# Performance work log

Measured on AMD Instinct MI355X. Metric: run time of the kernel, lower is better.

The kernel has to match this reference:

```python
import jax, jax.numpy as jnp
import numpy as np

N_NODES = 50000
N_EDGES = 625000
D = 128          # hidden_dim
H = 8            # num_heads
DH = D // H      # head_dim
L = 4            # num_layers
F_IN = 64        # in_channels
G = 64           # num graphs
BETA = 1.0
EPS = 1e-5       # layernorm eps


def _seg_softmax(s, idx, n):
    # softmax of s over segments defined by idx (segments present in idx are never empty)
    m = jax.ops.segment_max(s, idx, num_segments=n)
    e = jnp.exp(s - m[idx])
    d = jax.ops.segment_sum(e, idx, num_segments=n)
    return e / d[idx]


def _ln(x, s, b):
    mu = jnp.mean(x, axis=-1, keepdims=True)
    var = jnp.var(x, axis=-1, keepdims=True)
    return (x - mu) / jnp.sqrt(var + EPS) * s + b


def _forward(x, edge_index, batch, node_W, node_b, cW1, cb1, cW2, cb2,
             qW, qb, kW, kb, vW, vb, oW, ob, bW, bb,
             f1W, f1b, f2W, f2b, n1s, n1b, n2s, n2b,
             outW1, outb1, outW2, outb2):
    N = x.shape[0]
    src, tgt = edge_index[0], edge_index[1]
    h = x @ node_W + node_b                              # [N, D]
    for l in range(L):
        # ---- dynamic curvature (attention-approximated Wasserstein) ----
        h_src, h_tgt = h[src], h[tgt]                    # [E, D]
        sim = jnp.sum(h_src * h_tgt, axis=-1) * BETA     # [E]
        alpha = _seg_softmax(sim, tgt, N)                # segment softmax over tgt
        dist = jnp.linalg.norm(h_src - h_tgt, axis=-1)   # [E]
        agg = jax.ops.segment_sum(alpha * dist, tgt, num_segments=N)
        curv = 1.0 - agg[tgt] / jnp.maximum(dist, 1e-6)  # [E]
        ce = jax.nn.relu(curv[:, None] @ cW1 + cb1) @ cW2 + cb2  # [E, D]
        # ---- CurvphormerLayer ----
        xn = _ln(h, n1s[l], n1b[l])
        q = (xn @ qW[l] + qb[l]).reshape(N, H, DH)
        k = (xn @ kW[l] + kb[l]).reshape(N, H, DH)
        v = (xn @ vW[l] + vb[l]).reshape(N, H, DH)
        scores = jnp.sum(q[src] * k[tgt], axis=-1) / (DH ** 0.5)  # [E, H]
        scores = scores + ce @ bW[l] + bb[l]                       # curvature bias
        probs = _seg_softmax(scores, tgt, N)                       # [E, H]
        msgs = (probs[..., None] * v[tgt]).reshape(-1, D)          # [E, D]
        aggm = jax.ops.segment_sum(msgs, src, num_segments=N)     # scatter to src
        h = h + (aggm @ oW[l] + ob[l])
        xn2 = _ln(h, n2s[l], n2b[l])
        h = h + (jax.nn.relu(xn2 @ f1W[l] + f1b[l]) @ f2W[l] + f2b[l])
    # ---- mean pool per graph ----
    counts = jnp.maximum(jax.ops.segment_sum(jnp.ones((N,), h.dtype), batch, num_segments=G), 1.0)
    g = jax.ops.segment_sum(h, batch, num_segments=G) / counts[:, None]
    return jax.nn.relu(g @ outW1 + outb1) @ outW2 + outb2


def setup_inputs() -> dict:
    keys = iter(jax.random.split(jax.random.key(0), 32))
    p = lambda shape, s=0.02: jax.random.normal(next(keys), shape, jnp.float32) * s
    x = jax.random.normal(next(keys), (N_NODES, F_IN), jnp.float32)
    edge_index = jax.random.randint(next(keys), (2, N_EDGES), 0, N_NODES)
    batch = jnp.sort(jax.random.randint(next(keys), (N_NODES,), 0, G))
    inp = {
        "x": x, "edge_index": edge_index, "batch": batch,
        "node_W": p((F_IN, D)), "node_b": p((D,)),
        "cW1": p((1, D)), "cb1": p((D,)), "cW2": p((D, D)), "cb2": p((D,)),
        "qW": p((L, D, D)), "qb": p((L, D)),
        "kW": p((L, D, D)), "kb": p((L, D)),
        "vW": p((L, D, D)), "vb": p((L, D)),
        "oW": p((L, D, D)), "ob": p((L, D)),
        "bW": p((L, D, H)), "bb": p((L, H)),
        "f1W": p((L, D, 4 * D)), "f1b": p((L, 4 * D)),
        "f2W": p((L, 4 * D, D)), "f2b": p((L, D)),
        "n1s": jnp.ones((L, D), jnp.float32), "n1b": jnp.zeros((L, D), jnp.float32),
        "n2s": jnp.ones((L, D), jnp.float32), "n2b": jnp.zeros((L, D), jnp.float32),
        "outW1": p((D, D // 2)), "outb1": p((D // 2,)),
        "outW2": p((D // 2, 1)), "outb2": p((1,)),
    }
    return inp


def reference(x, edge_index, batch, node_W, node_b, cW1, cb1, cW2, cb2,
              qW, qb, kW, kb, vW, vb, oW, ob, bW, bb,
              f1W, f1b, f2W, f2b, n1s, n1b, n2s, n2b,
              outW1, outb1, outW2, outb2):
    return _forward(x, edge_index, batch, node_W, node_b, cW1, cb1, cW2, cb2,
                    qW, qb, kW, kb, vW, vb, oW, ob, bW, bb,
                    f1W, f1b, f2W, f2b, n1s, n1b, n2s, n2b,
                    outW1, outb1, outW2, outb2)
```

## Files before the change

kernel.cpp:

```cpp
#include <hip/hip_runtime.h>

#define NN 50000
#define NE 625000
#define DD 128
#define HH 8
#define DHH 16
#define NL 4
#define FIN 64
#define NG 64
#define LN_EPS 1e-5f
#define NSEG 129
#define NT32 1563
#define NT64 782
#define NBS 196
#define HLP 132

typedef __bf16 bf16x8_t __attribute__((ext_vector_type(8)));
typedef unsigned short ushort8_t __attribute__((ext_vector_type(8)));
typedef float f32x4_t __attribute__((ext_vector_type(4)));
union BF8 { ushort8_t u; bf16x8_t b; };

__device__ __forceinline__ void fma4(float4& a, float s, float4 w) {
  a.x = fmaf(s, w.x, a.x); a.y = fmaf(s, w.y, a.y);
  a.z = fmaf(s, w.z, a.z); a.w = fmaf(s, w.w, a.w);
}
__device__ __forceinline__ unsigned short f2bf(float f) {
  unsigned u = __float_as_uint(f);
  unsigned r = ((u >> 16) & 1u) + 0x7FFFu;
  return (unsigned short)((u + r) >> 16);
}
__device__ __forceinline__ float bf2f(unsigned short u) {
  return __uint_as_float((unsigned)u << 16);
}

__device__ __forceinline__ void ln_tile_bf32(const float* __restrict__ h, int nb,
                                             const float* __restrict__ sc,
                                             const float* __restrict__ bi,
                                             ushort* xbf) {
  int tid = threadIdx.x;
  int r = tid >> 4, l16 = tid & 15;
  int nr = nb + r; if (nr >= NN) nr = NN - 1;
  const float* hp = h + (size_t)nr * DD + l16 * 8;
  float4 a0 = *(const float4*)hp;
  float4 a1 = *(const float4*)(hp + 4);
  float sum = a0.x + a0.y + a0.z + a0.w + a1.x + a1.y + a1.z + a1.w;
  float sq  = a0.x*a0.x + a0.y*a0.y + a0.z*a0.z + a0.w*a0.w
            + a1.x*a1.x + a1.y*a1.y + a1.z*a1.z + a1.w*a1.w;
#pragma unroll
  for (int off = 8; off >= 1; off >>= 1) {
    sum += __shfl_xor(sum, off, 64);
    sq  += __shfl_xor(sq,  off, 64);
  }
  float mu   = sum * (1.0f / DD);
  float var  = sq * (1.0f / DD) - mu * mu;
  float rstd = rsqrtf(var + LN_EPS);
  int d0 = l16 * 8;
  float4 s0 = *(const float4*)(sc + d0), s1 = *(const float4*)(sc + d0 + 4);
  float4 b0 = *(const float4*)(bi + d0), b1 = *(const float4*)(bi + d0 + 4);
  ushort8_t u;
  u[0] = f2bf((a0.x - mu) * rstd * s0.x + b0.x);
  u[1] = f2bf((a0.y - mu) * rstd * s0.y + b0.y);
  u[2] = f2bf((a0.z - mu) * rstd * s0.z + b0.z);
  u[3] = f2bf((a0.w - mu) * rstd * s0.w + b0.w);
  u[4] = f2bf((a1.x - mu) * rstd * s1.x + b1.x);
  u[5] = f2bf((a1.y - mu) * rstd * s1.y + b1.y);
  u[6] = f2bf((a1.z - mu) * rstd * s1.z + b1.z);
  u[7] = f2bf((a1.w - mu) * rstd * s1.w + b1.w);
  int off = (r * 256 + l16 * 16) ^ ((r & 7) << 4);
  *(ushort8_t*)((char*)xbf + off) = u;
}

__global__ __launch_bounds__(256) void k_node_proj(const float* __restrict__ x,
                                                   const float* __restrict__ W,
                                                   const float* __restrict__ b,
                                                   float* __restrict__ h) {
  __shared__ float Wl[FIN * DD];
  __shared__ float xt[32][FIN];
  int tid = threadIdx.x;
  int nb = blockIdx.x * 32;
  for (int i = tid * 4; i < FIN * DD; i += 1024)
    *(float4*)&Wl[i] = *(const float4*)(W + i);
  for (int i = tid * 4; i < 32 * FIN; i += 1024) {
    int row = i >> 6, cc = i & 63;
    int node = nb + row; if (node >= NN) node = NN - 1;
    *(float4*)&xt[row][cc] = *(const float4*)(x + (size_t)node * FIN + cc);
  }
  __syncthreads();
  int c4 = (tid & 31) * 4;
  int r0 = (tid >> 5) * 4;
  float4 bv = *(const float4*)(b + c4);
  float4 a0 = bv, a1 = bv, a2 = bv, a3 = bv;
  for (int k = 0; k < FIN; k++) {
    float4 wv = *(const float4*)&Wl[k * DD + c4];
    fma4(a0, xt[r0][k], wv);
    fma4(a1, xt[r0 + 1][k], wv);
    fma4(a2, xt[r0 + 2][k], wv);
    fma4(a3, xt[r0 + 3][k], wv);
  }
  int n0 = nb + r0;
  if (n0 < NN)     *(float4*)(h + (size_t)n0 * DD + c4) = a0;
  if (n0 + 1 < NN) *(float4*)(h + (size_t)(n0 + 1) * DD + c4) = a1;
  if (n0 + 2 < NN) *(float4*)(h + (size_t)(n0 + 2) * DD + c4) = a2;
  if (n0 + 3 < NN) *(float4*)(h + (size_t)(n0 + 3) * DD + c4) = a3;
}

__global__ __launch_bounds__(256) void k_edge1(const int* __restrict__ src_s, const int* __restrict__ tgt_s,
                                               const float* __restrict__ h, float* __restrict__ sim,
                                               float* __restrict__ dist) {
  int gid = blockIdx.x * 256 + threadIdx.x;
  int e = gid >> 4;
  if (e >= NE) return;
  int j = gid & 15;
  int s = src_s[e], t = tgt_s[e];
  const float4* ap = (const float4*)(h + (size_t)s * DD + j * 8);
  const float4* bp = (const float4*)(h + (size_t)t * DD + j * 8);
  float4 a0 = ap[0], a1 = ap[1];
  float4 b0 = bp[0], b1 = bp[1];
  float dot = 0.f, sq = 0.f;
  dot = fmaf(a0.x, b0.x, dot); dot = fmaf(a0.y, b0.y, dot);
  dot = fmaf(a0.z, b0.z, dot); dot = fmaf(a0.w, b0.w, dot);
  dot = fmaf(a1.x, b1.x, dot); dot = fmaf(a1.y, b1.y, dot);
  dot = fmaf(a1.z, b1.z, dot); dot = fmaf(a1.w, b1.w, dot);
  float d0 = a0.x - b0.x, d1 = a0.y - b0.y, d2 = a0.z - b0.z, d3 = a0.w - b0.w;
  float d4 = a1.x - b1.x, d5 = a1.y - b1.y, d6 = a1.z - b1.z, d7 = a1.w - b1.w;
  sq = fmaf(d0, d0, sq); sq = fmaf(d1, d1, sq); sq = fmaf(d2, d2, sq); sq = fmaf(d3, d3, sq);
  sq = fmaf(d4, d4, sq); sq = fmaf(d5, d5, sq); sq = fmaf(d6, d6, sq); sq = fmaf(d7, d7, sq);
#pragma unroll
  for (int off = 8; off >= 1; off >>= 1) {
    dot += __shfl_xor(dot, off, 64);
    sq  += __shfl_xor(sq,  off, 64);
  }
  if (j == 0) {
    sim[e]  = dot;
    dist[e] = sqrtf(sq);
  }
}

__global__ __launch_bounds__(256) void k_curva(const int* __restrict__ rowstart_t,
    const int* __restrict__ eid_t, const float* __restrict__ sim,
    const float* __restrict__ dist, float* __restrict__ aggv) {
  int node = blockIdx.x * 32 + (threadIdx.x >> 3);
  if (node >= NN) return;
  int j = threadIdx.x & 7;
  int rs = rowstart_t[node], re = rowstart_t[node + 1];
  float m = -3.4e38f;
  for (int i = rs + j; i < re; i += 8) m = fmaxf(m, sim[eid_t[i]]);
#pragma unroll
  for (int off = 1; off <= 4; off <<= 1) m = fmaxf(m, __shfl_xor(m, off, 64));
  float den = 0.f, nd = 0.f;
  for (int i = rs + j; i < re; i += 8) {
    int e = eid_t[i];
    float ev = expf(sim[e] - m);
    den += ev;
    nd = fmaf(ev, dist[e], nd);
  }
#pragma unroll
  for (int off = 1; off <= 4; off <<= 1) {
    den += __shfl_xor(den, off, 64);
    nd  += __shfl_xor(nd,  off, 64);
  }
  if (j == 0) aggv[node] = den > 0.f ? nd / den : 0.f;
}

__global__ __launch_bounds__(512) void k_ln_qkv(const float* __restrict__ h,
    const float* __restrict__ n1s_l, const float* __restrict__ n1b_l,
    const ushort* __restrict__ qkvT_l,
    const float* __restrict__ qb_l, const float* __restrict__ kb_l, const float* __restrict__ vb_l,
    ushort* __restrict__ q, ushort* __restrict__ kk, ushort* __restrict__ v) {
  __shared__ __align__(16) ushort xbf[32 * DD];
  int nb = blockIdx.x * 32;
  ln_tile_bf32(h, nb, n1s_l, n1b_l, xbf);
  __syncthreads();
  int lane = threadIdx.x & 63;
  int w = threadIdx.x >> 6;
  int g = lane >> 4, c = lane & 15;
  int xr = (c & 7) << 4;
  char* xb = (char*)xbf;
  BF8 a[2][4];
#pragma unroll
  for (int nt = 0; nt < 2; nt++)
#pragma unroll
    for (int kt = 0; kt < 4; kt++)
      a[nt][kt].u = *(ushort8_t*)(xb + (((nt * 16 + c) * 256 + kt * 64 + g * 16) ^ xr));
#pragma unroll
  for (int ti = 0; ti < 3; ti++) {
    int t = w * 3 + ti;
    int m = t >> 3;
    int colb = (t & 7) * 16;
    const float* bias = (m == 0 ? qb_l : (m == 1 ? kb_l : vb_l));
    float4 bv = *(const float4*)(bias + colb + g * 4);
    f32x4_t acc0 = {bv.x, bv.y, bv.z, bv.w};
    f32x4_t acc1 = acc0;
    const ushort* wp = qkvT_l + (size_t)(m * DD + colb + c) * DD + g * 8;
#pragma unroll
    for (int kt = 0; kt < 4; kt++) {
      BF8 b; b.u = *(const ushort8_t*)(wp + kt * 32);
      acc0 = __builtin_amdgcn_mfma_f32_16x16x32_bf16(b.b, a[0][kt].b, acc0, 0, 0, 0);
      acc1 = __builtin_amdgcn_mfma_f32_16x16x32_bf16(b.b, a[1][kt].b, acc1, 0, 0, 0);
    }
    ushort* out = (m == 0 ? q : (m == 1 ? kk : v));
    int n0 = nb + c;
    if (n0 < NN) {
      ushort4 o; o.x = f2bf(acc0[0]); o.y = f2bf(acc0[1]); o.z = f2bf(acc0[2]); o.w = f2bf(acc0[3]);
      *(ushort4*)(out + (size_t)n0 * DD + colb + g * 4) = o;
    }
    int n1 = nb + 16 + c;
    if (n1 < NN) {
      ushort4 o; o.x = f2bf(acc1[0]); o.y = f2bf(acc1[1]); o.z = f2bf(acc1[2]); o.w = f2bf(acc1[3]);
      *(ushort4*)(out + (size_t)n1 * DD + colb + g * 4) = o;
    }
  }
}

__global__ __launch_bounds__(256) void k_scores_sm(const int* __restrict__ src_s,
    const int* __restrict__ rowstart_t, const int* __restrict__ eid_t,
    const ushort* __restrict__ q, const ushort* __restrict__ k,
    const float* __restrict__ dist, const float* __restrict__ aggv,
    const float* __restrict__ bp_g,
    const float* __restrict__ slope_l, const float* __restrict__ inter_l,
    float* __restrict__ escore, float2* __restrict__ msd) {
  __shared__ float lsl[NSEG * HH], lin[NSEG * HH], bp[DD];
  int tid = threadIdx.x;
  for (int idx = tid; idx < NSEG * HH; idx += 256) { lsl[idx] = slope_l[idx]; lin[idx] = inter_l[idx]; }
  if (tid < DD) bp[tid] = bp_g[tid];
  __syncthreads();
  int node = blockIdx.x * 32 + (tid >> 3);
  if (node >= NN) return;
  int hh = tid & 7;
  int rs = rowstart_t[node], re = rowstart_t[node + 1];
  float av = aggv[node];
  const ushort8_t* kp = (const ushort8_t*)(k + (size_t)node * DD + hh * DHH);
  ushort8_t k0 = kp[0], k1 = kp[1];
  float m = -3.4e38f;
  int i = rs;
  int e_n = 0, s_n = 0; float dd_n = 0.f; ushort8_t q0_n = {}, q1_n = {};
  if (i < re) {
    e_n = eid_t[i]; s_n = src_s[e_n]; dd_n = dist[e_n];
    const ushort8_t* qp = (const ushort8_t*)(q + (size_t)s_n * DD + hh * DHH);
    q0_n = qp[0]; q1_n = qp[1];
  }
  while (i < re) {
    int e = e_n; float dd = dd_n;
    ushort8_t q0 = q0_n, q1 = q1_n;
    int j = i + 1;
    if (j < re) {
      e_n = eid_t[j]; s_n = src_s[e_n]; dd_n = dist[e_n];
      const ushort8_t* qp = (const ushort8_t*)(q + (size_t)s_n * DD + hh * DHH);
      q0_n = qp[0]; q1_n = qp[1];
    }
    float curv = 1.0f - av / fmaxf(dd, 1e-6f);
    int lo = 0, hi = DD;
    while (lo < hi) { int mid = (lo + hi) >> 1; if (bp[mid] < curv) lo = mid + 1; else hi = mid; }
    float bias = fmaf(lsl[lo * HH + hh], curv, lin[lo * HH + hh]);
    float dot = 0.f;
#pragma unroll
    for (int jj = 0; jj < 8; jj++) dot = fmaf(bf2f(q0[jj]), bf2f(k0[jj]), dot);
#pragma unroll
    for (int jj = 0; jj < 8; jj++) dot = fmaf(bf2f(q1[jj]), bf2f(k1[jj]), dot);
    float sc = dot * 0.25f + bias;
    escore[e * HH + hh] = sc;
    m = fmaxf(m, sc);
    i = j;
  }
  float sum = 0.f;
  for (i = rs; i < re; i++)
    sum += expf(escore[eid_t[i] * HH + hh] - m);
  float2 o; o.x = m; o.y = sum > 0.f ? 1.0f / sum : 0.f;
  msd[(size_t)node * HH + hh] = o;
}

__global__ __launch_bounds__(256) void k_agg(const int* __restrict__ tgt_s,
    const int* __restrict__ rowstart,
    const float* __restrict__ escore, const float2* __restrict__ msd,
    const ushort* __restrict__ v, ushort* __restrict__ aggmb) {
  int wave = (blockIdx.x * 256 + threadIdx.x) >> 6;
  int lane = threadIdx.x & 63;
  int rs = rowstart[wave], re = rowstart[wave + 1];
  int hh = lane >> 3;
  int d = lane * 2;
  float a0 = 0.f, a1 = 0.f;
  int i = rs;
  for (; i + 4 <= re; i += 4) {
    int t0 = tgt_s[i], t1 = tgt_s[i + 1], t2 = tgt_s[i + 2], t3 = tgt_s[i + 3];
    float e0 = escore[(i    ) * HH + hh];
    float e1 = escore[(i + 1) * HH + hh];
    float e2 = escore[(i + 2) * HH + hh];
    float e3 = escore[(i + 3) * HH + hh];
    float2 m0 = msd[(size_t)t0 * HH + hh], m1 = msd[(size_t)t1 * HH + hh];
    float2 m2 = msd[(size_t)t2 * HH + hh], m3 = msd[(size_t)t3 * HH + hh];
    ushort2 v0 = *(const ushort2*)(v + (size_t)t0 * DD + d);
    ushort2 v1 = *(const ushort2*)(v + (size_t)t1 * DD + d);
    ushort2 v2 = *(const ushort2*)(v + (size_t)t2 * DD + d);
    ushort2 v3 = *(const ushort2*)(v + (size_t)t3 * DD + d);
    float p0 = expf(e0 - m0.x) * m0.y;
    float p1 = expf(e1 - m1.x) * m1.y;
    float p2 = expf(e2 - m2.x) * m2.y;
    float p3 = expf(e3 - m3.x) * m3.y;
    a0 = fmaf(p0, bf2f(v0.x), a0); a1 = fmaf(p0, bf2f(v0.y), a1);
    a0 = fmaf(p1, bf2f(v1.x), a0); a1 = fmaf(p1, bf2f(v1.y), a1);
    a0 = fmaf(p2, bf2f(v2.x), a0); a1 = fmaf(p2, bf2f(v2.y), a1);
    a0 = fmaf(p3, bf2f(v3.x), a0); a1 = fmaf(p3, bf2f(v3.y), a1);
  }
  for (; i < re; i++) {
    int t = tgt_s[i];
    float2 md = msd[(size_t)t * HH + hh];
    float prob = expf(escore[i * HH + hh] - md.x) * md.y;
    ushort2 vv = *(const ushort2*)(v + (size_t)t * DD + d);
    a0 = fmaf(prob, bf2f(vv.x), a0);
    a1 = fmaf(prob, bf2f(vv.y), a1);
  }
  ushort2 o; o.x = f2bf(a0); o.y = f2bf(a1);
  *(ushort2*)(aggmb + (size_t)wave * DD + d) = o;
}

__global__ __launch_bounds__(512) void k_attn_ffn(const ushort* __restrict__ aggmb,
    const ushort* __restrict__ oT_l, const float* __restrict__ ob_l,
    const float* __restrict__ n2s_l, const float* __restrict__ n2b_l,
    const ushort* __restrict__ f1T_l, const float* __restrict__ f1b_l,
    const ushort* __restrict__ f2T_l, const float* __restrict__ f2b_l,
    float* __restrict__ h) {
  __shared__ float hL[64 * HLP];
  __shared__ __align__(16) char ubuf[64 * 256 * 2];
  char* xb = ubuf;
  char* tb = ubuf;
  int nb = blockIdx.x * 64;
  int tid = threadIdx.x;
  int lane = tid & 63, w = tid >> 6;
  int g = lane >> 4, c = lane & 15;
  int colb = w * 16;
  int xr = (c & 7) << 4;
  {
    float4 obv = *(const float4*)(ob_l + colb + g * 4);
    const ushort* wp = oT_l + (size_t)(colb + c) * DD + g * 8;
    BF8 b0, b1, b2, b3;
    b0.u = *(const ushort8_t*)(wp);
    b1.u = *(const ushort8_t*)(wp + 32);
    b2.u = *(const ushort8_t*)(wp + 64);
    b3.u = *(const ushort8_t*)(wp + 96);
#pragma unroll
    for (int nt = 0; nt < 4; nt++) {
      int node = nb + nt * 16 + c;
      int na = node < NN ? node : NN - 1;
      const ushort* ap = aggmb + (size_t)na * DD + g * 8;
      BF8 a0, a1, a2, a3;
      a0.u = *(const ushort8_t*)(ap);
      a1.u = *(const ushort8_t*)(ap + 32);
      a2.u = *(const ushort8_t*)(ap + 64);
      a3.u = *(const ushort8_t*)(ap + 96);
      f32x4_t acc = {obv.x, obv.y, obv.z, obv.w};
      acc = __builtin_amdgcn_mfma_f32_16x16x32_bf16(b0.b, a0.b, acc, 0, 0, 0);
      acc = __builtin_amdgcn_mfma_f32_16x16x32_bf16(b1.b, a1.b, acc, 0, 0, 0);
      acc = __builtin_amdgcn_mfma_f32_16x16x32_bf16(b2.b, a2.b, acc, 0, 0, 0);
      acc = __builtin_amdgcn_mfma_f32_16x16x32_bf16(b3.b, a3.b, acc, 0, 0, 0);
      float4 hv = *(const float4*)(h + (size_t)na * DD + colb + g * 4);
      hv.x += acc[0]; hv.y += acc[1]; hv.z += acc[2]; hv.w += acc[3];
      *(float4*)&hL[(nt * 16 + c) * HLP + colb + g * 4] = hv;
    }
  }
  __syncthreads();
  {
    int l16 = tid & 15;
    int d0 = l16 * 8;
    float4 s0 = *(const float4*)(n2s_l + d0), s1 = *(const float4*)(n2s_l + d0 + 4);
    float4 bb0 = *(const float4*)(n2b_l + d0), bb1 = *(const float4*)(n2b_l + d0 + 4);
#pragma unroll
    for (int p = 0; p < 2; p++) {
      int r = p * 32 + (tid >> 4);
      const float* hp = &hL[r * HLP + d0];
      float4 a0 = *(const float4*)hp;
      float4 a1 = *(const float4*)(hp + 4);
      float sum = a0.x + a0.y + a0.z + a0.w + a1.x + a1.y + a1.z + a1.w;
      float sq  = a0.x*a0.x + a0.y*a0.y + a0.z*a0.z + a0.w*a0.w
                + a1.x*a1.x + a1.y*a1.y + a1.z*a1.z + a1.w*a1.w;
#pragma unroll
      for (int off = 8; off >= 1; off >>= 1) {
        sum += __shfl_xor(sum, off, 64);
        sq  += __shfl_xor(sq,  off, 64);
      }
      float mu   = sum * (1.0f / DD);
      float var  = sq * (1.0f / DD) - mu * mu;
      float rstd = rsqrtf(var + LN_EPS);
      ushort8_t u;
      u[0] = f2bf((a0.x - mu) * rstd * s0.x + bb0.x);
      u[1] = f2bf((a0.y - mu) * rstd * s0.y + bb0.y);
      u[2] = f2bf((a0.z - mu) * rstd * s0.z + bb0.z);
      u[3] = f2bf((a0.w - mu) * rstd * s0.w + bb0.w);
      u[4] = f2bf((a1.x - mu) * rstd * s1.x + bb1.x);
      u[5] = f2bf((a1.y - mu) * rstd * s1.y + bb1.y);
      u[6] = f2bf((a1.z - mu) * rstd * s1.z + bb1.z);
      u[7] = f2bf((a1.w - mu) * rstd * s1.w + bb1.w);
      int off = (r * 256 + l16 * 16) ^ ((r & 7) << 4);
      *(ushort8_t*)(xb + off) = u;
    }
  }
  __syncthreads();
  BF8 a[4][4];
#pragma unroll
  for (int nt = 0; nt < 4; nt++)
#pragma unroll
    for (int kt = 0; kt < 4; kt++)
      a[nt][kt].u = *(ushort8_t*)(xb + (((nt * 16 + c) * 256 + kt * 64 + g * 16) ^ xr));
  __syncthreads();
  float4 bv2 = *(const float4*)(f2b_l + colb + g * 4);
  f32x4_t o0 = {bv2.x, bv2.y, bv2.z, bv2.w};
  f32x4_t o1 = o0, o2 = o0, o3 = o0;
#pragma unroll
  for (int ch = 0; ch < 2; ch++) {
    if (ch) __syncthreads();
#pragma unroll
    for (int ti = 0; ti < 2; ti++) {
      int ctile = w * 2 + ti;
      int col = ch * 256 + ctile * 16;
      float4 bv = *(const float4*)(f1b_l + col + g * 4);
      f32x4_t ac0 = {bv.x, bv.y, bv.z, bv.w};
      f32x4_t ac1 = ac0, ac2 = ac0, ac3 = ac0;
      const ushort* wp = f1T_l + (size_t)(col + c) * DD + g * 8;
#pragma unroll
      for (int kt = 0; kt < 4; kt++) {
        BF8 b; b.u = *(const ushort8_t*)(wp + kt * 32);
        ac0 = __builtin_amdgcn_mfma_f32_16x16x32_bf16(b.b, a[0][kt].b, ac0, 0, 0, 0);
        ac1 = __builtin_amdgcn_mfma_f32_16x16x32_bf16(b.b, a[1][kt].b, ac1, 0, 0, 0);
        ac2 = __builtin_amdgcn_mfma_f32_16x16x32_bf16(b.b, a[2][kt].b, ac2, 0, 0, 0);
        ac3 = __builtin_amdgcn_mfma_f32_16x16x32_bf16(b.b, a[3][kt].b, ac3, 0, 0, 0);
      }
      int colL = (ctile * 16 + g * 4) * 2;
      {
        int row = c;
        ushort4 o4; o4.x = f2bf(fmaxf(ac0[0], 0.f)); o4.y = f2bf(fmaxf(ac0[1], 0.f));
        o4.z = f2bf(fmaxf(ac0[2], 0.f)); o4.w = f2bf(fmaxf(ac0[3], 0.f));
        *(ushort4*)(tb + ((row * 512 + colL) ^ ((row & 7) << 4))) = o4;
      }
      {
        int row = 16 + c;
        ushort4 o4; o4.x = f2bf(fmaxf(ac1[0], 0.f)); o4.y = f2bf(fmaxf(ac1[1], 0.f));
        o4.z = f2bf(fmaxf(ac1[2], 0.f)); o4.w = f2bf(fmaxf(ac1[3], 0.f));
        *(ushort4*)(tb + ((row * 512 + colL) ^ ((row & 7) << 4))) = o4;
      }
      {
        int row = 32 + c;
        ushort4 o4; o4.x = f2bf(fmaxf(ac2[0], 0.f)); o4.y = f2bf(fmaxf(ac2[1], 0.f));
        o4.z = f2bf(fmaxf(ac2[2], 0.f)); o4.w = f2bf(fmaxf(ac2[3], 0.f));
        *(ushort4*)(tb + ((row * 512 + colL) ^ ((row & 7) << 4))) = o4;
      }
      {
        int row = 48 + c;
        ushort4 o4; o4.x = f2bf(fmaxf(ac3[0], 0.f)); o4.y = f2bf(fmaxf(ac3[1], 0.f));
        o4.z = f2bf(fmaxf(ac3[2], 0.f)); o4.w = f2bf(fmaxf(ac3[3], 0.f));
        *(ushort4*)(tb + ((row * 512 + colL) ^ ((row & 7) << 4))) = o4;
      }
    }
    __syncthreads();
    const ushort* wp2 = f2T_l + (size_t)(colb + c) * 512 + ch * 256 + g * 8;
#pragma unroll
    for (int kt = 0; kt < 8; kt++) {
      BF8 b; b.u = *(const ushort8_t*)(wp2 + kt * 32);
      BF8 t0; t0.u = *(ushort8_t*)(tb + (((c) * 512 + kt * 64 + g * 16) ^ xr));
      BF8 t1; t1.u = *(ushort8_t*)(tb + (((16 + c) * 512 + kt * 64 + g * 16) ^ xr));
      BF8 t2; t2.u = *(ushort8_t*)(tb + (((32 + c) * 512 + kt * 64 + g * 16) ^ xr));
      BF8 t3; t3.u = *(ushort8_t*)(tb + (((48 + c) * 512 + kt * 64 + g * 16) ^ xr));
      o0 = __builtin_amdgcn_mfma_f32_16x16x32_bf16(b.b, t0.b, o0, 0, 0, 0);
      o1 = __builtin_amdgcn_mfma_f32_16x16x32_bf16(b.b, t1.b, o1, 0, 0, 0);
      o2 = __builtin_amdgcn_mfma_f32_16x16x32_bf16(b.b, t2.b, o2, 0, 0, 0);
      o3 = __builtin_amdgcn_mfma_f32_16x16x32_bf16(b.b, t3.b, o3, 0, 0, 0);
    }
  }
  {
    int node = nb + c;
    if (node < NN) {
      const float* lp = &hL[c * HLP + colb + g * 4];
      float4 hv = *(const float4*)lp;
      hv.x += o0[0]; hv.y += o0[1]; hv.z += o0[2]; hv.w += o0[3];
      *(float4*)(h + (size_t)node * DD + colb + g * 4) = hv;
    }
  }
  {
    int node = nb + 16 + c;
    if (node < NN) {
      const float* lp = &hL[(16 + c) * HLP + colb + g * 4];
      float4 hv = *(const float4*)lp;
      hv.x += o1[0]; hv.y += o1[1]; hv.z += o1[2]; hv.w += o1[3];
      *(float4*)(h + (size_t)node * DD + colb + g * 4) = hv;
    }
  }
  {
    int node = nb + 32 + c;
    if (node < NN) {
      const float* lp = &hL[(32 + c) * HLP + colb + g * 4];
      float4 hv = *(const float4*)lp;
      hv.x += o2[0]; hv.y += o2[1]; hv.z += o2[2]; hv.w += o2[3];
      *(float4*)(h + (size_t)node * DD + colb + g * 4) = hv;
    }
  }
  {
    int node = nb + 48 + c;
    if (node < NN) {
      const float* lp = &hL[(48 + c) * HLP + colb + g * 4];
      float4 hv = *(const float4*)lp;
      hv.x += o3[0]; hv.y += o3[1]; hv.z += o3[2]; hv.w += o3[3];
      *(float4*)(h + (size_t)node * DD + colb + g * 4) = hv;
    }
  }
}

template <int K, int C>
__global__ void k_wt(const float* __restrict__ W, ushort* __restrict__ WT, int nm, int dstride) {
  int idx = blockIdx.x * 256 + threadIdx.x;
  if (idx >= K * C * nm) return;
  int mi = idx / (K * C), rem = idx - mi * (K * C);
  int cc = rem / K, kk2 = rem - cc * K;
  WT[(size_t)mi * dstride + cc * K + kk2] = f2bf(W[(size_t)mi * K * C + (size_t)kk2 * C + cc]);
}

__global__ void k_hist(const int* __restrict__ idxs, int* __restrict__ cnt) {
  int e = blockIdx.x * 256 + threadIdx.x;
  if (e < NE) atomicAdd(cnt + idxs[e], 1);
}

__global__ __launch_bounds__(256) void k_scan_blk(const int* __restrict__ cnt, int* __restrict__ bsum) {
  __shared__ int red[256];
  int tid = threadIdx.x;
  int idx = blockIdx.x * 256 + tid;
  red[tid] = (idx < NN) ? cnt[idx] : 0;
  __syncthreads();
  for (int off = 128; off >= 1; off >>= 1) {
    if (tid < off) red[tid] += red[tid + off];
    __syncthreads();
  }
  if (tid == 0) bsum[blockIdx.x] = red[0];
}

__global__ __launch_bounds__(256) void k_scan_top(const int* __restrict__ bsum,
                                                  int* __restrict__ boff, int* __restrict__ rowstart) {
  __shared__ int ps[256];
  int t = threadIdx.x;
  int v = (t < NBS) ? bsum[t] : 0;
  ps[t] = v;
  __syncthreads();
  for (int off = 1; off < 256; off <<= 1) {
    int x = (t >= off) ? ps[t - off] : 0;
    __syncthreads();
    ps[t] += x;
    __syncthreads();
  }
  boff[t] = ps[t] - v;
  if (t == 255) rowstart[NN] = ps[255];
}

__global__ __launch_bounds__(256) void k_scan_fin(const int* __restrict__ cnt,
                                                  const int* __restrict__ boff, int* __restrict__ rowstart) {
  __shared__ int ps[256];
  int t = threadIdx.x;
  int idx = blockIdx.x * 256 + t;
  int v = (idx < NN) ? cnt[idx] : 0;
  ps[t] = v;
  __syncthreads();
  for (int off = 1; off < 256; off <<= 1) {
    int x = (t >= off) ? ps[t - off] : 0;
    __syncthreads();
    ps[t] += x;
    __syncthreads();
  }
  if (idx < NN) rowstart[idx] = boff[blockIdx.x] + ps[t] - v;
}

__global__ void k_fill(const int* __restrict__ src, const int* __restrict__ tgt,
                       const int* __restrict__ rowstart,
                       int* __restrict__ cur, int* __restrict__ src_s, int* __restrict__ tgt_s) {
  int e = blockIdx.x * 256 + threadIdx.x;
  if (e >= NE) return;
  int s = src[e];
  int p = atomicAdd(cur + s, 1);
  int pos = rowstart[s] + p;
  src_s[pos] = s;
  tgt_s[pos] = tgt[e];
}

__global__ void k_fill_t(const int* __restrict__ tgt_s, const int* __restrict__ rowstart_t,
                         int* __restrict__ cur_t, int* __restrict__ eid_t) {
  int i = blockIdx.x * 256 + threadIdx.x;
  if (i >= NE) return;
  int t = tgt_s[i];
  int p = atomicAdd(cur_t + t, 1);
  eid_t[rowstart_t[t] + p] = i;
}

__global__ __launch_bounds__(64) void k_mbias_par(const float* __restrict__ cW2, const float* __restrict__ cb2,
                                                  const float* __restrict__ bW, const float* __restrict__ bb,
                                                  float* __restrict__ M, float* __restrict__ base) {
  int bid = blockIdx.x;
  int l = bid >> 7, d = bid & 127;
  int lane = threadIdx.x;
  int hh = lane >> 3, j0 = lane & 7;
  const float* bWl = bW + (size_t)l * DD * HH;
  float acc = 0.f;
#pragma unroll
  for (int t = 0; t < 16; t++) {
    int k = j0 + t * 8;
    acc = fmaf(cW2[d * DD + k], bWl[k * HH + hh], acc);
  }
#pragma unroll
  for (int off = 1; off <= 4; off <<= 1) acc += __shfl_xor(acc, off, 64);
  if (j0 == 0) M[(size_t)l * DD * HH + d * HH + hh] = acc;
  if (d == 0) {
    float bacc = 0.f;
#pragma unroll
    for (int t = 0; t < 16; t++) {
      int k = j0 + t * 8;
      bacc = fmaf(cb2[k], bWl[k * HH + hh], bacc);
    }
#pragma unroll
    for (int off = 1; off <= 4; off <<= 1) bacc += __shfl_xor(bacc, off, 64);
    if (j0 == 0) base[l * HH + hh] = bacc + bb[l * HH + hh];
  }
}

__global__ __launch_bounds__(128) void k_bp(const float* __restrict__ cW1, const float* __restrict__ cb1,
                                            float* __restrict__ bpg, int* __restrict__ posg) {
  __shared__ float x[DD], bp[DD];
  int tid = threadIdx.x;
  float c1v = cW1[tid], cbv = cb1[tid];
  x[tid] = (c1v == 0.f) ? __builtin_inff() : (-cbv / c1v);
  __syncthreads();
  float xv = x[tid]; int p = 0;
  for (int j = 0; j < DD; j++) {
    float xj = x[j];
    if (xj < xv || (xj == xv && j < tid)) p++;
  }
  bp[p] = xv;
  posg[tid] = p;
  __syncthreads();
  bpg[tid] = bp[tid];
}

__global__ __launch_bounds__(64) void k_pwl_tab(const float* __restrict__ cW1, const float* __restrict__ cb1,
    const int* __restrict__ posg, const float* __restrict__ Mb, const float* __restrict__ basel,
    float* __restrict__ slopeg, float* __restrict__ interg) {
  int bid = blockIdx.x;
  int l = bid / NSEG, s = bid - l * NSEG;
  int lane = threadIdx.x;
  int hh = lane >> 3, j0 = lane & 7;
  const float* M = Mb + (size_t)l * DD * HH;
  float sl = 0.f, in = 0.f;
#pragma unroll
  for (int t = 0; t < 16; t++) {
    int d = j0 + t * 8;
    float cv = cW1[d], cbv = cb1[d];
    int p = posg[d];
    bool act = (cv == 0.f) ? (cbv > 0.f) : ((cv > 0.f) ? (p < s) : (p >= s));
    float m = act ? M[d * HH + hh] : 0.f;
    sl = fmaf(cv, m, sl);
    in = fmaf(cbv, m, in);
  }
#pragma unroll
  for (int off = 1; off <= 4; off <<= 1) {
    sl += __shfl_xor(sl, off, 64);
    in += __shfl_xor(in, off, 64);
  }
  if (j0 == 0) {
    size_t o = (size_t)l * NSEG * HH + s * HH + hh;
    slopeg[o] = sl;
    interg[o] = in + basel[l * HH + hh];
  }
}

__global__ void k_bounds(const int* __restrict__ batch, int* __restrict__ gstart, int* __restrict__ gend) {
  int n = blockIdx.x * 256 + threadIdx.x;
  if (n >= NN) return;
  int b = batch[n];
  if (n == 0 || batch[n - 1] != b) gstart[b] = n;
  if (n == NN - 1 || batch[n + 1] != b) gend[b] = n + 1;
}

__global__ __launch_bounds__(256) void k_pool_part(const float* __restrict__ h,
    const int* __restrict__ batch, float* __restrict__ gpool) {
  int tid = threadIdx.x;
  int d = tid & 127, sub = tid >> 7;
  int n0 = blockIdx.x * 256;
  int nend = n0 + 256; if (nend > NN) nend = NN;
  float run = 0.f; int gcur = -1;
  for (int n = n0 + sub; n < nend; n += 2) {
    int g = batch[n];
    if (g != gcur) {
      if (gcur >= 0) atomicAdd(gpool + (size_t)gcur * DD + d, run);
      run = 0.f; gcur = g;
    }
    run += h[(size_t)n * DD + d];
  }
  if (gcur >= 0) atomicAdd(gpool + (size_t)gcur * DD + d, run);
}

__global__ __launch_bounds__(256) void k_head(const float* __restrict__ gpool,
    const int* __restrict__ gstart, const int* __restrict__ gend,
    const float* __restrict__ W1, const float* __restrict__ b1,
    const float* __restrict__ W2, const float* __restrict__ b2, float* __restrict__ out) {
  __shared__ float mid[NG * 64];
  int tid = threadIdx.x;
  for (int idx = tid; idx < NG * 64; idx += 256) {
    int g = idx >> 6, j = idx & 63;
    int cnt = gend[g] - gstart[g]; if (cnt < 1) cnt = 1;
    float rc = 1.0f / (float)cnt;
    float acc = 0.f;
    for (int d = 0; d < DD; d++) acc = fmaf(gpool[g * DD + d], W1[d * 64 + j], acc);
    mid[idx] = fmaxf(fmaf(acc, rc, b1[j]), 0.f);
  }
  __syncthreads();
  if (tid < NG) {
    float acc = b2[0];
    for (int j = 0; j < 64; j++) acc = fmaf(mid[tid * 64 + j], W2[j], acc);
    out[tid] = acc;
  }
}

extern "C" void kernel_launch(void* const* d_in, const int* in_sizes, int n_in,
                              void* d_out, int out_size, void* d_ws, size_t ws_size,
                              hipStream_t stream) {
  const float* x      = (const float*)d_in[0];
  const int*   ei     = (const int*)d_in[1];
  const int*   batch  = (const int*)d_in[2];
  const float* node_W = (const float*)d_in[3];
  const float* node_b = (const float*)d_in[4];
  const float* cW1    = (const float*)d_in[5];
  const float* cb1    = (const float*)d_in[6];
  const float* cW2    = (const float*)d_in[7];
  const float* cb2    = (const float*)d_in[8];
  const float* qW     = (const float*)d_in[9];
  const float* qb     = (const float*)d_in[10];
  const float* kW     = (const float*)d_in[11];
  const float* kb     = (const float*)d_in[12];
  const float* vW     = (const float*)d_in[13];
  const float* vb     = (const float*)d_in[14];
  const float* oW     = (const float*)d_in[15];
  const float* ob     = (const float*)d_in[16];
  const float* bW     = (const float*)d_in[17];
  const float* bb     = (const float*)d_in[18];
  const float* f1W    = (const float*)d_in[19];
  const float* f1b    = (const float*)d_in[20];
  const float* f2W    = (const float*)d_in[21];
  const float* f2b    = (const float*)d_in[22];
  const float* n1s    = (const float*)d_in[23];
  const float* n1b    = (const float*)d_in[24];
  const float* n2s    = (const float*)d_in[25];
  const float* n2b    = (const float*)d_in[26];
  const float* outW1  = (const float*)d_in[27];
  const float* outb1  = (const float*)d_in[28];
  const float* outW2  = (const float*)d_in[29];
  const float* outb2  = (const float*)d_in[30];

  const int* src = ei;
  const int* tgt = ei + NE;

  char* wp = (char*)d_ws;
  auto alloc = [&](size_t bytes) { void* p = (void*)wp; wp += (bytes + 255) & ~(size_t)255; return p; };
  float*    h       = (float*)alloc((size_t)NN * DD * 4);
  ushort*   q       = (ushort*)alloc((size_t)NN * DD * 2);
  ushort*   kk      = (ushort*)alloc((size_t)NN * DD * 2);
  ushort*   v       = (ushort*)alloc((size_t)NN * DD * 2);
  ushort*   aggmb   = (ushort*)alloc((size_t)NN * DD * 2);
  float*    sim     = (float*)alloc((size_t)NE * 4);
  float*    dist    = (float*)alloc((size_t)NE * 4);
  float*    escore  = (float*)alloc((size_t)NE * HH * 4);
  float2*   msd     = (float2*)alloc((size_t)NN * HH * 8);
  float*    aggv    = (float*)alloc((size_t)NN * 4);
  float*    Mb      = (float*)alloc((size_t)NL * DD * HH * 4);
  float*    basel   = (float*)alloc((size_t)NL * HH * 4);
  float*    bpg     = (float*)alloc((size_t)DD * 4);
  int*      posg    = (int*)alloc((size_t)DD * 4);
  float*    slopeg  = (float*)alloc((size_t)NL * NSEG * HH * 4);
  float*    interg  = (float*)alloc((size_t)NL * NSEG * HH * 4);
  int*      rowstart= (int*)alloc((size_t)(NN + 1) * 4);
  int*      rowstart_t = (int*)alloc((size_t)(NN + 1) * 4);
  int*      eid_t   = (int*)alloc((size_t)NE * 4);
  int*      src_s   = (int*)alloc((size_t)NE * 4);
  int*      tgt_s   = (int*)alloc((size_t)NE * 4);
  int*      cnt     = (int*)alloc((size_t)NN * 4);
  int*      cur     = (int*)alloc((size_t)NN * 4);
  int*      cnt_t   = (int*)alloc((size_t)NN * 4);
  int*      cur_t   = (int*)alloc((size_t)NN * 4);
  int*      bsum    = (int*)alloc((size_t)NBS * 4);
  int*      boff    = (int*)alloc((size_t)256 * 4);
  int*      gstart  = (int*)alloc((size_t)NG * 4);
  int*      gend    = (int*)alloc((size_t)NG * 4);
  float*    gpool   = (float*)alloc((size_t)NG * DD * 4);
  ushort*   qkvT    = (ushort*)alloc((size_t)NL * 3 * DD * DD * 2);
  ushort*   oT      = (ushort*)alloc((size_t)NL * DD * DD * 2);
  ushort*   f1T     = (ushort*)alloc((size_t)NL * DD * 512 * 2);
  ushort*   f2T     = (ushort*)alloc((size_t)NL * 512 * DD * 2);
  (void)in_sizes; (void)n_in; (void)out_size; (void)ws_size;

  hipMemsetAsync(cnt, 0, NN * 4, stream);
  hipMemsetAsync(cur, 0, NN * 4, stream);
  hipMemsetAsync(cnt_t, 0, NN * 4, stream);
  hipMemsetAsync(cur_t, 0, NN * 4, stream);
  hipMemsetAsync(gstart, 0, NG * 4, stream);
  hipMemsetAsync(gend, 0, NG * 4, stream);
  hipMemsetAsync(gpool, 0, NG * DD * 4, stream);
  k_hist<<<(NE + 255) / 256, 256, 0, stream>>>(src, cnt);
  k_scan_blk<<<NBS, 256, 0, stream>>>(cnt, bsum);
  k_scan_top<<<1, 256, 0, stream>>>(bsum, boff, rowstart);
  k_scan_fin<<<NBS, 256, 0, stream>>>(cnt, boff, rowstart);
  k_fill<<<(NE + 255) / 256, 256, 0, stream>>>(src, tgt, rowstart, cur, src_s, tgt_s);
  k_hist<<<(NE + 255) / 256, 256, 0, stream>>>(tgt, cnt_t);
  k_scan_blk<<<NBS, 256, 0, stream>>>(cnt_t, bsum);
  k_scan_top<<<1, 256, 0, stream>>>(bsum, boff, rowstart_t);
  k_scan_fin<<<NBS, 256, 0, stream>>>(cnt_t, boff, rowstart_t);
  k_fill_t<<<(NE + 255) / 256, 256, 0, stream>>>(tgt_s, rowstart_t, cur_t, eid_t);
  k_mbias_par<<<NL * DD, 64, 0, stream>>>(cW2, cb2, bW, bb, Mb, basel);
  k_bp<<<1, 128, 0, stream>>>(cW1, cb1, bpg, posg);
  k_pwl_tab<<<NL * NSEG, 64, 0, stream>>>(cW1, cb1, posg, Mb, basel, slopeg, interg);
  k_bounds<<<(NN + 255) / 256, 256, 0, stream>>>(batch, gstart, gend);
  k_wt<DD, DD><<<(NL * DD * DD + 255) / 256, 256, 0, stream>>>(qW, qkvT,               NL, 3 * DD * DD);
  k_wt<DD, DD><<<(NL * DD * DD + 255) / 256, 256, 0, stream>>>(kW, qkvT + DD * DD,     NL, 3 * DD * DD);
  k_wt<DD, DD><<<(NL * DD * DD + 255) / 256, 256, 0, stream>>>(vW, qkvT + 2 * DD * DD, NL, 3 * DD * DD);
  k_wt<DD, DD><<<(NL * DD * DD + 255) / 256, 256, 0, stream>>>(oW, oT, NL, DD * DD);
  k_wt<DD, 512><<<(NL * DD * 512 + 255) / 256, 256, 0, stream>>>(f1W, f1T, NL, DD * 512);
  k_wt<512, DD><<<(NL * DD * 512 + 255) / 256, 256, 0, stream>>>(f2W, f2T, NL, DD * 512);
  k_node_proj<<<NT32, 256, 0, stream>>>(x, node_W, node_b, h);

  for (int l = 0; l < NL; l++) {
    k_edge1<<<(NE * 16 + 255) / 256, 256, 0, stream>>>(src_s, tgt_s, h, sim, dist);
    k_curva<<<NT32, 256, 0, stream>>>(rowstart_t, eid_t, sim, dist, aggv);
    k_ln_qkv<<<NT32, 512, 0, stream>>>(h, n1s + l * DD, n1b + l * DD,
        qkvT + (size_t)l * 3 * DD * DD,
        qb + l * DD, kb + l * DD, vb + l * DD, q, kk, v);
    k_scores_sm<<<NT32, 256, 0, stream>>>(src_s, rowstart_t, eid_t, q, kk,
        dist, aggv, bpg,
        slopeg + (size_t)l * NSEG * HH, interg + (size_t)l * NSEG * HH,
        escore, msd);
    k_agg<<<NN / 4, 256, 0, stream>>>(tgt_s, rowstart, escore, msd, v, aggmb);
    k_attn_ffn<<<NT64, 512, 0, stream>>>(aggmb, oT + (size_t)l * DD * DD, ob + l * DD,
        n2s + l * DD, n2b + l * DD,
        f1T + (size_t)l * DD * 512, f1b + (size_t)l * 4 * DD,
        f2T + (size_t)l * 512 * DD, f2b + l * DD, h);
  }
  k_pool_part<<<(NN + 255) / 256, 256, 0, stream>>>(h, batch, gpool);
  k_head<<<1, 256, 0, stream>>>(gpool, gstart, gend, outW1, outb1, outW2, outb2, (float*)d_out);
}
```

Measured before the change: 1.407 ms.

## Parallelize score kernel across edges per node with online softmax reduction

The scores kernel now assigns a full 64-lane wave per target node, with 8 lanes per head striding over that node's incoming edges, instead of one thread per (node, head) walking edges serially. The separate second pass that re-read escore to compute the softmax denominator is replaced by an online max/sum, merged across lanes with xor shuffles. This raises memory-level parallelism for the gathered q rows and removes a dependent re-read pass. The cost is 8x more blocks, each reloading the 129x8 slope/intercept tables into shared memory, which is a large per-block setup relative to the small amount of edge work per node. It also adds extra exp evaluations per edge.

Result: faster. 1.322 ms (-6.1%).

```diff
diff --git a/kernel.cpp b/kernel.cpp
--- a/kernel.cpp
+++ b/kernel.cpp
@@ -12,6 +12,7 @@
 #define NSEG 129
 #define NT32 1563
 #define NT64 782
+#define NT4 12500
 #define NBS 196
 #define HLP 132
 
@@ -224,30 +225,22 @@
   for (int idx = tid; idx < NSEG * HH; idx += 256) { lsl[idx] = slope_l[idx]; lin[idx] = inter_l[idx]; }
   if (tid < DD) bp[tid] = bp_g[tid];
   __syncthreads();
-  int node = blockIdx.x * 32 + (tid >> 3);
+  int node = blockIdx.x * 4 + (tid >> 6);
   if (node >= NN) return;
-  int hh = tid & 7;
+  int lane = tid & 63;
+  int hh = lane & 7;
+  int eidx = lane >> 3;
   int rs = rowstart_t[node], re = rowstart_t[node + 1];
   float av = aggv[node];
   const ushort8_t* kp = (const ushort8_t*)(k + (size_t)node * DD + hh * DHH);
   ushort8_t k0 = kp[0], k1 = kp[1];
-  float m = -3.4e38f;
-  int i = rs;
-  int e_n = 0, s_n = 0; float dd_n = 0.f; ushort8_t q0_n = {}, q1_n = {};
-  if (i < re) {
-    e_n = eid_t[i]; s_n = src_s[e_n]; dd_n = dist[e_n];
-    const ushort8_t* qp = (const ushort8_t*)(q + (size_t)s_n * DD + hh * DHH);
-    q0_n = qp[0]; q1_n = qp[1];
-  }
-  while (i < re) {
-    int e = e_n; float dd = dd_n;
-    ushort8_t q0 = q0_n, q1 = q1_n;
-    int j = i + 1;
-    if (j < re) {
-      e_n = eid_t[j]; s_n = src_s[e_n]; dd_n = dist[e_n];
-      const ushort8_t* qp = (const ushort8_t*)(q + (size_t)s_n * DD + hh * DHH);
-      q0_n = qp[0]; q1_n = qp[1];
-    }
+  float m = -3.4e38f, ssum = 0.f;
+  for (int i = rs + eidx; i < re; i += 8) {
+    int e = eid_t[i];
+    int s = src_s[e];
+    float dd = dist[e];
+    const ushort8_t* qp = (const ushort8_t*)(q + (size_t)s * DD + hh * DHH);
+    ushort8_t q0 = qp[0], q1 = qp[1];
     float curv = 1.0f - av / fmaxf(dd, 1e-6f);
     int lo = 0, hi = DD;
     while (lo < hi) { int mid = (lo + hi) >> 1; if (bp[mid] < curv) lo = mid + 1; else hi = mid; }
@@ -259,14 +252,22 @@
     for (int jj = 0; jj < 8; jj++) dot = fmaf(bf2f(q1[jj]), bf2f(k1[jj]), dot);
     float sc = dot * 0.25f + bias;
     escore[e * HH + hh] = sc;
-    m = fmaxf(m, sc);
-    i = j;
-  }
-  float sum = 0.f;
-  for (i = rs; i < re; i++)
-    sum += expf(escore[eid_t[i] * HH + hh] - m);
-  float2 o; o.x = m; o.y = sum > 0.f ? 1.0f / sum : 0.f;
-  msd[(size_t)node * HH + hh] = o;
+    float mn = fmaxf(m, sc);
+    ssum = ssum * expf(m - mn) + expf(sc - mn);
+    m = mn;
+  }
+#pragma unroll
+  for (int off = 8; off <= 32; off <<= 1) {
+    float m2 = __shfl_xor(m, off, 64);
+    float s2 = __shfl_xor(ssum, off, 64);
+    float M = fmaxf(m, m2);
+    ssum = ssum * expf(m - M) + s2 * expf(m2 - M);
+    m = M;
+  }
+  if (eidx == 0) {
+    float2 o; o.x = m; o.y = ssum > 0.f ? 1.0f / ssum : 0.f;
+    msd[(size_t)node * HH + hh] = o;
+  }
 }
 
 __global__ __launch_bounds__(256) void k_agg(const int* __restrict__ tgt_s,
@@ -822,7 +823,7 @@
     k_ln_qkv<<<NT32, 512, 0, stream>>>(h, n1s + l * DD, n1b + l * DD,
         qkvT + (size_t)l * 3 * DD * DD,
         qb + l * DD, kb + l * DD, vb + l * DD, q, kk, v);
-    k_scores_sm<<<NT32, 256, 0, stream>>>(src_s, rowstart_t, eid_t, q, kk,
+    k_scores_sm<<<NT4, 256, 0, stream>>>(src_s, rowstart_t, eid_t, q, kk,
         dist, aggv, bpg,
         slopeg + (size_t)l * NSEG * HH, interg + (size_t)l * NSEG * HH,
         escore, msd);
```
